# Kernel tuning notes

Hardware: AMD Instinct MI355X
Metric: run time of the kernel (lower is better)

The kernel has to match this reference:

```python
import jax, jax.numpy as jnp
import numpy as np

E = 8
HIDDEN = 1024
INTER = 4096
CAPS = np.array([512, 1024, 2048, 4096, 1024, 512, 2048, 1024], dtype=np.int64)  # sum = 12288
TOTAL = int(CAPS.sum())


def setup_inputs() -> dict:
    key = jax.random.key(0)
    k1, k2, k3, k4, k5 = jax.random.split(key, 5)
    s1 = 1.0 / np.sqrt(HIDDEN)
    s2 = 1.0 / np.sqrt(INTER)
    return {
        "inter_state": jax.random.normal(k1, (TOTAL, HIDDEN), dtype=jnp.float32),
        "w1": jax.random.normal(k2, (E, INTER, HIDDEN), dtype=jnp.float32) * s1,
        "b1": jax.random.normal(k3, (E, INTER), dtype=jnp.float32) * s1,
        "w2": jax.random.normal(k4, (E, HIDDEN, INTER), dtype=jnp.float32) * s2,
        "b2": jax.random.normal(k5, (E, HIDDEN), dtype=jnp.float32) * s2,
        "capacities": jnp.asarray(CAPS),
    }


def reference(inter_state, w1, b1, w2, b2, capacities):
    # Grouped GEMM: tokens are contiguous per expert with sizes = capacities.
    # Capacities are routing metadata (static for slicing).
    caps = np.asarray(capacities)
    offs = np.concatenate([[0], np.cumsum(caps)]).astype(np.int64)
    outs = []
    for e in range(caps.shape[0]):  # small fixed expert loop
        x = inter_state[int(offs[e]):int(offs[e + 1])]      # [cap_e, hidden]
        h = x @ w1[e].T + b1[e]                              # [cap_e, inter]
        outs.append(h @ w2[e].T + b2[e])                     # [cap_e, hidden]
    return jnp.concatenate(outs, axis=0)                     # [total, hidden]
```

## Files before the change

### kernel.cpp

```cpp
#include <hip/hip_runtime.h>
#include <hip/hip_bf16.h>

#define DEV __device__ __forceinline__

typedef __bf16 bf16x8 __attribute__((ext_vector_type(8)));
typedef float  f32x4  __attribute__((ext_vector_type(4)));


DEV unsigned short f2bf(float f) {
  union { float f; unsigned u; } v; v.f = f;
  unsigned u = v.u;
  return (unsigned short)((u + 0x7FFFu + ((u >> 16) & 1u)) >> 16);
}

DEV float bf2f(unsigned short s) {
  union { unsigned u; float f; } v; v.u = (unsigned)s << 16; return v.f;
}

DEV void gld_lds16(const void* g, void* l) {
  __builtin_amdgcn_global_load_lds(
      (const __attribute__((address_space(1))) unsigned int*)g,
      (__attribute__((address_space(3))) unsigned int*)l, 16, 0, 0);
}

#define WAITVM(N) asm volatile("s_waitcnt vmcnt(" #N ")" ::: "memory"); \
                  __builtin_amdgcn_sched_barrier(0)
#define WAITLG(N) asm volatile("s_waitcnt lgkmcnt(" #N ")" ::: "memory"); \
                  __builtin_amdgcn_sched_barrier(0)

template <int KT_, int KLEN, int SK, int N_, int NCT, bool OUT_BF16,
          bool HAS_BIAS, int EDIV>
__global__ __launch_bounds__(512, 2)
void gemm256(const unsigned short* __restrict__ A,
             const unsigned short* __restrict__ B,
             const float* __restrict__ bias,
             void* __restrict__ C0, void* __restrict__ C1) {
  __shared__ __align__(128) char lds[2][65536];
  constexpr int NTILES = KLEN / 64;

  const int tid  = threadIdx.x;
  const int lane = tid & 63;
  const int wv   = tid >> 6;
  const int wm   = wv >> 2;
  const int wn   = wv & 3;
  const int fr   = lane & 15;
  const int fq   = lane >> 4;

  int bid = blockIdx.x;
  const int nwg = gridDim.x;
  bid = (bid & 7) * (nwg >> 3) + (bid >> 3);

  int sk = 0;
  if constexpr (SK > 1) {
    const int per = nwg / SK;
    sk = bid / per;
    bid -= sk * per;
  }
  const int kStart = sk * KLEN;
  void* Cv = (SK > 1 && sk == 1) ? C1 : C0;

  const int rt = bid / NCT;
  const int ct = bid - rt * NCT;

  int e;
  if constexpr (EDIV > 0) {
    e = rt / EDIV;
  } else {
    const int cums[9] = {0, 2, 6, 14, 30, 34, 36, 44, 48};
    e = 0;
#pragma unroll
    for (int i = 1; i < 8; ++i) e += (rt >= cums[i]) ? 1 : 0;
  }

  const int grow0 = rt * 256;
  const int nloc0 = ct * 256;
  const unsigned short* Bg = B + (size_t)e * N_ * KT_;

  f32x4 acc[8][4];
#pragma unroll
  for (int i = 0; i < 8; ++i)
#pragma unroll
    for (int j = 0; j < 4; ++j) acc[i][j] = (f32x4){0.f, 0.f, 0.f, 0.f};

  auto stage_half = [&](int buf, int tk2, int h) {
    const int kb = kStart + tk2 * 64;
    char* dst = lds[buf] + h * 16384;
    const unsigned short* src = (h < 2) ? A : Bg;
    const int row0 = (h < 2) ? (grow0 + h * 128) : (nloc0 + (h - 2) * 128);
#pragma unroll
    for (int s = 0; s < 2; ++s) {
      int o  = s * 8192 + wv * 1024 + lane * 16;
      int r  = o >> 7;
      int cb = (o & 127) ^ ((r & 7) << 4);
      gld_lds16(src + (size_t)(row0 + r) * KT_ + kb + (cb >> 1),
                dst + s * 8192 + wv * 1024);
    }
  };

  stage_half(0, 0, 0); stage_half(0, 0, 1);
  stage_half(0, 0, 2); stage_half(0, 0, 3);

  const int brow0 = (wn & 1) * 64;

  for (int tk = 0; tk < NTILES; ++tk) {
    const int cur = tk & 1;
    WAITVM(0);
    __builtin_amdgcn_s_barrier();
    __builtin_amdgcn_sched_barrier(0);

    char* Ah = lds[cur] + wm * 16384;
    char* Bh = lds[cur] + (2 + (wn >> 1)) * 16384;
    const bool pre = (tk + 1 < NTILES);

    bf16x8 bfr[4][2], afr[2][2];
#pragma unroll
    for (int ni = 0; ni < 4; ++ni) {
      int r = brow0 + ni * 16 + fr;
#pragma unroll
      for (int k = 0; k < 2; ++k)
        bfr[ni][k] = *(bf16x8*)(Bh + r * 128 + ((k * 64 + fq * 16) ^ ((r & 7) << 4)));
    }
#pragma unroll
    for (int j = 0; j < 2; ++j) {
      int r = j * 16 + fr;
#pragma unroll
      for (int k = 0; k < 2; ++k)
        afr[j][k] = *(bf16x8*)(Ah + r * 128 + ((k * 64 + fq * 16) ^ ((r & 7) << 4)));
    }
    if (pre) { stage_half(cur ^ 1, tk + 1, 0); stage_half(cur ^ 1, tk + 1, 1); }
    WAITLG(0);
    __builtin_amdgcn_s_setprio(1);
#pragma unroll
    for (int k = 0; k < 2; ++k)
#pragma unroll
      for (int j = 0; j < 2; ++j)
#pragma unroll
        for (int ni = 0; ni < 4; ++ni)
          acc[j][ni] = __builtin_amdgcn_mfma_f32_16x16x32_bf16(
              afr[j][k], bfr[ni][k], acc[j][ni], 0, 0, 0);
    __builtin_amdgcn_s_setprio(0);

#pragma unroll
    for (int q = 1; q < 4; ++q) {
#pragma unroll
      for (int j = 0; j < 2; ++j) {
        int r = (2 * q + j) * 16 + fr;
#pragma unroll
        for (int k = 0; k < 2; ++k)
          afr[j][k] = *(bf16x8*)(Ah + r * 128 + ((k * 64 + fq * 16) ^ ((r & 7) << 4)));
      }
      if (q == 1 && pre) { stage_half(cur ^ 1, tk + 1, 2); stage_half(cur ^ 1, tk + 1, 3); }
      WAITLG(0);
      __builtin_amdgcn_s_setprio(1);
#pragma unroll
      for (int k = 0; k < 2; ++k)
#pragma unroll
        for (int j = 0; j < 2; ++j)
#pragma unroll
          for (int ni = 0; ni < 4; ++ni)
            acc[2 * q + j][ni] = __builtin_amdgcn_mfma_f32_16x16x32_bf16(
                afr[j][k], bfr[ni][k], acc[2 * q + j][ni], 0, 0, 0);
      __builtin_amdgcn_s_setprio(0);
    }
  }

#pragma unroll
  for (int ni = 0; ni < 4; ++ni) {
    int ncol = nloc0 + wn * 64 + ni * 16 + fr;
    float bv = 0.f;
    if constexpr (HAS_BIAS) bv = (bias + (size_t)e * N_)[ncol];
#pragma unroll
    for (int mi = 0; mi < 8; ++mi) {
      int m = grow0 + wm * 128 + mi * 16 + fq * 4;
#pragma unroll
      for (int j = 0; j < 4; ++j) {
        float val = acc[mi][ni][j] + bv;
        if constexpr (OUT_BF16)
          ((unsigned short*)Cv)[(size_t)(m + j) * N_ + ncol] = f2bf(val);
        else
          ((float*)Cv)[(size_t)(m + j) * N_ + ncol] = val;
      }
    }
  }
}

__global__ __launch_bounds__(256)
void reduce_bf16(const unsigned short* __restrict__ p0,
                 const unsigned short* __restrict__ p1,
                 unsigned short* __restrict__ out, int n8) {
  for (int i = blockIdx.x * 256 + threadIdx.x; i < n8; i += gridDim.x * 256) {
    ushort4 a0 = ((const ushort4*)p0)[2 * i];
    ushort4 a1 = ((const ushort4*)p0)[2 * i + 1];
    ushort4 b0 = ((const ushort4*)p1)[2 * i];
    ushort4 b1 = ((const ushort4*)p1)[2 * i + 1];
    ushort4 r0 = {f2bf(bf2f(a0.x) + bf2f(b0.x)), f2bf(bf2f(a0.y) + bf2f(b0.y)),
                  f2bf(bf2f(a0.z) + bf2f(b0.z)), f2bf(bf2f(a0.w) + bf2f(b0.w))};
    ushort4 r1 = {f2bf(bf2f(a1.x) + bf2f(b1.x)), f2bf(bf2f(a1.y) + bf2f(b1.y)),
                  f2bf(bf2f(a1.z) + bf2f(b1.z)), f2bf(bf2f(a1.w) + bf2f(b1.w))};
    ((ushort4*)out)[2 * i]     = r0;
    ((ushort4*)out)[2 * i + 1] = r1;
  }
}

DEV int swz(int r, int cbyte) {
  return (r * 64 + cbyte) ^ (((r >> 1) & 7) << 4);
}

template <int K_, int N_, bool OUT_BF16, bool HAS_BIAS, int EDIV>
__global__ __launch_bounds__(512, 2)
void gemm8(const unsigned short* __restrict__ A,
           const unsigned short* __restrict__ B,
           const float* __restrict__ bias, void* __restrict__ Cv) {
  __shared__ __align__(128) char lds[2][49152];
  const int t    = threadIdx.x;
  const int lane = t & 63;
  const int wv   = t >> 6;
  const int wm   = wv >> 1;
  const int wn   = wv & 1;
  const int fr   = lane & 15;
  const int fq   = lane >> 4;
  constexpr int NCT = N_ / 128;
  constexpr int NT  = K_ / 64;

  int bid = blockIdx.x;
  const int nwg = gridDim.x;
  bid = (bid & 7) * (nwg >> 3) + (bid >> 3);
  const int rt = bid / NCT;
  const int ct = bid - rt * NCT;

  int e;
  if constexpr (EDIV > 0) {
    e = rt / EDIV;
  } else {
    const int cums[9] = {0, 2, 6, 14, 30, 34, 36, 44, 48};
    e = 0;
#pragma unroll
    for (int i = 1; i < 8; ++i) e += (rt >= cums[i]) ? 1 : 0;
  }

  const int grow0 = rt * 256;
  const int nloc0 = ct * 128;
  const unsigned short* Bg = B + (size_t)e * N_ * K_;

  f32x4 acc[4][4];
#pragma unroll
  for (int i = 0; i < 4; ++i)
#pragma unroll
    for (int j = 0; j < 4; ++j) acc[i][j] = (f32x4){0.f, 0.f, 0.f, 0.f};

  auto stage = [&](int buf, int tk) {
    const int kb = tk * 64;
    char* Abase = lds[buf];
    char* Bbase = lds[buf] + 32768;
#pragma unroll
    for (int s = 0; s < 4; ++s) {
      int o  = s * 8192 + wv * 1024 + lane * 16;
      int r  = o >> 7;
      int cb = (o & 127) ^ ((r & 7) << 4);
      gld_lds16(A + (size_t)(grow0 + r) * K_ + kb + (cb >> 1),
                Abase + s * 8192 + wv * 1024);
    }
#pragma unroll
    for (int s = 0; s < 2; ++s) {
      int o  = s * 8192 + wv * 1024 + lane * 16;
      int r  = o >> 7;
      int cb = (o & 127) ^ ((r & 7) << 4);
      gld_lds16(Bg + (size_t)(nloc0 + r) * K_ + kb + (cb >> 1),
                Bbase + s * 8192 + wv * 1024);
    }
  };

  auto compute = [&](int buf) {
    char* Abase = lds[buf];
    char* Bbase = lds[buf] + 32768;
    bf16x8 af[4][2], bf[4][2];
#pragma unroll
    for (int mi = 0; mi < 4; ++mi) {
      int r = wm * 64 + mi * 16 + fr;
#pragma unroll
      for (int k = 0; k < 2; ++k)
        af[mi][k] = *(bf16x8*)(Abase + r * 128 + ((k * 64 + fq * 16) ^ ((r & 7) << 4)));
    }
#pragma unroll
    for (int ni = 0; ni < 4; ++ni) {
      int r = wn * 64 + ni * 16 + fr;
#pragma unroll
      for (int k = 0; k < 2; ++k)
        bf[ni][k] = *(bf16x8*)(Bbase + r * 128 + ((k * 64 + fq * 16) ^ ((r & 7) << 4)));
    }
    __builtin_amdgcn_s_setprio(1);
#pragma unroll
    for (int k = 0; k < 2; ++k)
#pragma unroll
      for (int mi = 0; mi < 4; ++mi)
#pragma unroll
        for (int ni = 0; ni < 4; ++ni)
          acc[mi][ni] = __builtin_amdgcn_mfma_f32_16x16x32_bf16(
              af[mi][k], bf[ni][k], acc[mi][ni], 0, 0, 0);
    __builtin_amdgcn_s_setprio(0);
  };

  stage(0, 0);
  for (int tk = 0; tk < NT; ++tk) {
    const int cur = tk & 1;
    if (tk + 1 < NT) {
      stage(cur ^ 1, tk + 1);
      WAITVM(6);
    } else {
      WAITVM(0);
    }
    __builtin_amdgcn_s_barrier();
    compute(cur);
    WAITLG(0);
    __builtin_amdgcn_s_barrier();
  }

#pragma unroll
  for (int ni = 0; ni < 4; ++ni) {
    int nloc = nloc0 + wn * 64 + ni * 16 + fr;
    float bv = 0.f;
    if constexpr (HAS_BIAS) bv = (bias + (size_t)e * N_)[nloc];
#pragma unroll
    for (int mi = 0; mi < 4; ++mi) {
      int m = grow0 + wm * 64 + mi * 16 + fq * 4;
#pragma unroll
      for (int j = 0; j < 4; ++j) {
        float val = acc[mi][ni][j] + bv;
        if constexpr (OUT_BF16)
          ((unsigned short*)Cv)[(size_t)(m + j) * N_ + nloc] = f2bf(val);
        else
          ((float*)Cv)[(size_t)(m + j) * N_ + nloc] = val;
      }
    }
  }
}

template <int K_, int N_, int NCT_, bool OUT_BF16, bool HAS_BIAS, int EDIV>
__global__ __launch_bounds__(256)
void gemm_expert(const void* __restrict__ Av, const void* __restrict__ Bv,
                 const float* __restrict__ bias, void* __restrict__ Cv) {
  __shared__ char lds[2][12288];
  const int t    = threadIdx.x;
  const int lane = t & 63;
  const int wv   = t >> 6;
  const int wr   = wv >> 1;
  const int wc   = wv & 1;
  const int fr   = lane & 15;
  const int fq   = lane >> 4;

  int bid = blockIdx.x;
  const int nwg = gridDim.x;
  if ((nwg & 7) == 0) bid = (bid & 7) * (nwg >> 3) + (bid >> 3);
  const int rt = bid / NCT_;
  const int ct = bid - rt * NCT_;

  int e;
  if constexpr (EDIV > 0) {
    e = rt / EDIV;
  } else {
    const int cums[9] = {0, 4, 12, 28, 60, 68, 72, 88, 96};
    e = 0;
#pragma unroll
    for (int i = 1; i < 8; ++i) e += (rt >= cums[i]) ? 1 : 0;
  }

  const int grow0 = rt * 128;
  const int nloc0 = ct * 64;

  f32x4 acc[4][2];
#pragma unroll
  for (int i = 0; i < 4; ++i)
#pragma unroll
    for (int j = 0; j < 2; ++j) acc[i][j] = (f32x4){0.f, 0.f, 0.f, 0.f};

  const float* Af = (const float*)Av;
  const unsigned short* Bb = (const unsigned short*)Bv + (size_t)e * N_ * K_;

  auto stage = [&](int buf, int kb) {
    char* As = lds[buf];
    char* Bs = lds[buf] + 8192;
#pragma unroll
    for (int it = 0; it < 4; ++it) {
      int q = t + it * 256, r = q >> 3, c = (q & 7) * 4;
      float4 f = *(const float4*)(Af + (size_t)(grow0 + r) * K_ + kb + c);
      ushort4 v = {f2bf(f.x), f2bf(f.y), f2bf(f.z), f2bf(f.w)};
      *(ushort4*)(As + swz(r, c * 2)) = v;
    }
    int o = wv * 1024 + lane * 16;
    int p = o ^ (((o >> 7) & 7) << 4);
    gld_lds16(Bb + (size_t)(nloc0 + (p >> 6)) * K_ + kb + ((p & 63) >> 1),
              Bs + wv * 1024);
  };

  auto compute = [&](int buf) {
    char* As = lds[buf];
    char* Bs = lds[buf] + 8192;
    bf16x8 af[4], bfg[2];
#pragma unroll
    for (int mi = 0; mi < 4; ++mi)
      af[mi] = *(bf16x8*)(As + swz(wr * 64 + mi * 16 + fr, fq * 16));
#pragma unroll
    for (int ni = 0; ni < 2; ++ni)
      bfg[ni] = *(bf16x8*)(Bs + swz(wc * 32 + ni * 16 + fr, fq * 16));
#pragma unroll
    for (int mi = 0; mi < 4; ++mi)
#pragma unroll
      for (int ni = 0; ni < 2; ++ni)
        acc[mi][ni] = __builtin_amdgcn_mfma_f32_16x16x32_bf16(
            af[mi], bfg[ni], acc[mi][ni], 0, 0, 0);
  };

  int cur = 0;
  stage(0, 0);
  __syncthreads();
  for (int kb = 32; kb < K_; kb += 32) {
    stage(cur ^ 1, kb);
    compute(cur);
    __syncthreads();
    cur ^= 1;
  }
  compute(cur);

#pragma unroll
  for (int ni = 0; ni < 2; ++ni) {
    int nloc = nloc0 + wc * 32 + ni * 16 + fr;
    float bv = 0.f;
    if constexpr (HAS_BIAS) bv = (bias + (size_t)e * N_)[nloc];
#pragma unroll
    for (int mi = 0; mi < 4; ++mi) {
      int m = grow0 + wr * 64 + mi * 16 + fq * 4;
#pragma unroll
      for (int j = 0; j < 4; ++j) {
        float val = acc[mi][ni][j] + bv;
        if constexpr (OUT_BF16)
          ((unsigned short*)Cv)[(size_t)(m + j) * N_ + nloc] = f2bf(val);
        else
          ((float*)Cv)[(size_t)(m + j) * N_ + nloc] = val;
      }
    }
  }
}

__global__ __launch_bounds__(256)
void transpose_w1(const float* __restrict__ w1, unsigned short* __restrict__ w1t) {
  __shared__ unsigned short tl[64 * 68];
  int b = blockIdx.x;
  int jt = b & 15, kt = (b >> 4) & 63, e = b >> 10;
  const float* src = w1 + ((size_t)e * 4096 + kt * 64) * 1024 + jt * 64;
  int t = threadIdx.x;
#pragma unroll
  for (int it = 0; it < 4; ++it) {
    int q = t + it * 256, kr = q >> 4, jc = (q & 15) * 4;
    float4 f = *(const float4*)(src + (size_t)kr * 1024 + jc);
    ushort4 v = {f2bf(f.x), f2bf(f.y), f2bf(f.z), f2bf(f.w)};
    *(ushort4*)&tl[kr * 68 + jc] = v;
  }
  __syncthreads();
  unsigned short* dst = w1t + ((size_t)e * 1024 + jt * 64) * 4096 + kt * 64;
#pragma unroll
  for (int it = 0; it < 4; ++it) {
    int q = t + it * 256, jr = q >> 4, kc = (q & 15) * 4;
    ushort4 v = {tl[(kc + 0) * 68 + jr], tl[(kc + 1) * 68 + jr],
                 tl[(kc + 2) * 68 + jr], tl[(kc + 3) * 68 + jr]};
    *(ushort4*)(dst + (size_t)jr * 4096 + kc) = v;
  }
}

template <bool STORE_BF>
__global__ __launch_bounds__(256)
void conv_w2_bias(const float* __restrict__ w2, const float* __restrict__ b1,
                  const float* __restrict__ b2, unsigned short* __restrict__ w2bf,
                  float* __restrict__ bc) {
  int row = blockIdx.x, e = row >> 10, t = threadIdx.x;
  const float* src = w2 + (size_t)row * 4096;
  const float* b1e = b1 + (size_t)e * 4096;
  float acc = 0.f;
#pragma unroll
  for (int it = 0; it < 4; ++it) {
    int c = (t + it * 256) * 4;
    float4 f = *(const float4*)(src + c);
    float4 g = *(const float4*)(b1e + c);
    acc += f.x * g.x + f.y * g.y + f.z * g.z + f.w * g.w;
    if constexpr (STORE_BF) {
      ushort4 v = {f2bf(f.x), f2bf(f.y), f2bf(f.z), f2bf(f.w)};
      *(ushort4*)(w2bf + (size_t)row * 4096 + c) = v;
    }
  }
#pragma unroll
  for (int o = 32; o > 0; o >>= 1) acc += __shfl_down(acc, o);
  __shared__ float red[4];
  if ((t & 63) == 0) red[t >> 6] = acc;
  __syncthreads();
  if (t == 0) bc[row] = red[0] + red[1] + red[2] + red[3] + b2[row];
}

__global__ __launch_bounds__(256)
void conv_f32_bf16(const float* __restrict__ in, unsigned short* __restrict__ out,
                   int n4) {
  for (int i = blockIdx.x * 256 + threadIdx.x; i < n4; i += gridDim.x * 256) {
    float4 f = *(const float4*)(in + (size_t)i * 4);
    ushort4 v = {f2bf(f.x), f2bf(f.y), f2bf(f.z), f2bf(f.w)};
    *(ushort4*)(out + (size_t)i * 4) = v;
  }
}

extern "C" void kernel_launch(void* const* d_in, const int* in_sizes, int n_in,
                              void* d_out, int out_size, void* d_ws, size_t ws_size,
                              hipStream_t stream) {
  const float* x  = (const float*)d_in[0];
  const float* w1 = (const float*)d_in[1];
  const float* b1 = (const float*)d_in[2];
  const float* w2 = (const float*)d_in[3];
  const float* b2 = (const float*)d_in[4];

  char* ws = (char*)d_ws;
  unsigned short* w1t = (unsigned short*)ws;
  const size_t NEED_T2 = 151126016, NEED_T3 = 176291840;

  if (ws_size >= NEED_T3) {
    unsigned short* w2bf = (unsigned short*)(ws + 67108864);
    unsigned short* Wc   = (unsigned short*)(ws + 134217728);
    float*          bc   = (float*)(ws + 150994944);
    unsigned short* xbf  = (unsigned short*)(ws + 151126016);
    unsigned short* p1   = xbf;

    transpose_w1<<<8192, 256, 0, stream>>>(w1, w1t);
    conv_w2_bias<true><<<8192, 256, 0, stream>>>(w2, b1, b2, w2bf, bc);
    gemm256<4096, 2048, 2, 1024, 4, true, false, 4>
        <<<256, 512, 0, stream>>>(w2bf, w1t, nullptr, Wc, p1);
    reduce_bf16<<<2048, 256, 0, stream>>>(Wc, p1, Wc, 8 * 1024 * 1024 / 8);
    conv_f32_bf16<<<2048, 256, 0, stream>>>(x, xbf, 12288 * 1024 / 4);
    gemm256<1024, 1024, 1, 1024, 4, false, true, 0>
        <<<192, 512, 0, stream>>>(xbf, Wc, bc, (float*)d_out, nullptr);
  } else if (ws_size >= NEED_T2) {
    unsigned short* w2bf = (unsigned short*)(ws + 67108864);
    unsigned short* Wc   = (unsigned short*)(ws + 134217728);
    float*          bc   = (float*)(ws + 150994944);

    transpose_w1<<<8192, 256, 0, stream>>>(w1, w1t);
    conv_w2_bias<true><<<8192, 256, 0, stream>>>(w2, b1, b2, w2bf, bc);
    gemm8<4096, 1024, true, false, 4>
        <<<256, 512, 0, stream>>>(w2bf, w1t, nullptr, Wc);
    gemm_expert<1024, 1024, 16, false, true, 0>
        <<<1536, 256, 0, stream>>>(x, Wc, bc, d_out);
  } else {
    unsigned short* Wc = (unsigned short*)(ws + 67108864);
    float*          bc = (float*)(ws + 83886080);

    transpose_w1<<<8192, 256, 0, stream>>>(w1, w1t);
    conv_w2_bias<false><<<8192, 256, 0, stream>>>(w2, b1, b2, nullptr, bc);
    gemm_expert<4096, 1024, 8, true, false, 8>
        <<<768, 256, 0, stream>>>(w2, w1t, nullptr, Wc);
    gemm_expert<1024, 1024, 16, false, true, 0>
        <<<1536, 256, 0, stream>>>(x, Wc, bc, d_out);
  }
}
```

Baseline: 205.0 us.

## Deepen GEMM prefetch pipeline with split A/B LDS buffers and partial waits

Reorganizes LDS into separate double-buffered A and B regions and prefetches B tiles two iterations ahead while A is prefetched one ahead. The per-iteration wait now uses a partial vmcnt instead of draining all loads, and a mid-iteration barrier lets the next tile's A overwrite safely. The intent is to hide global-load latency behind MFMA work in both GEMM stages, at the cost of an extra barrier per iteration and more complex buffer-reuse ordering.

```diff
diff --git a/kernel.cpp b/kernel.cpp
--- a/kernel.cpp
+++ b/kernel.cpp
@@ -27,16 +27,17 @@
                   __builtin_amdgcn_sched_barrier(0)
 #define WAITLG(N) asm volatile("s_waitcnt lgkmcnt(" #N ")" ::: "memory"); \
                   __builtin_amdgcn_sched_barrier(0)
+#define BARRIER() __builtin_amdgcn_s_barrier(); __builtin_amdgcn_sched_barrier(0)
 
 template <int KT_, int KLEN, int SK, int N_, int NCT, bool OUT_BF16,
           bool HAS_BIAS, int EDIV>
 __global__ __launch_bounds__(512, 2)
-void gemm256(const unsigned short* __restrict__ A,
-             const unsigned short* __restrict__ B,
-             const float* __restrict__ bias,
-             void* __restrict__ C0, void* __restrict__ C1) {
-  __shared__ __align__(128) char lds[2][65536];
-  constexpr int NTILES = KLEN / 64;
+void gemm256p(const unsigned short* __restrict__ A,
+              const unsigned short* __restrict__ B,
+              const float* __restrict__ bias,
+              void* __restrict__ C0, void* __restrict__ C1) {
+  __shared__ __align__(128) char lds[131072];
+  constexpr int NT = KLEN / 64;
 
   const int tid  = threadIdx.x;
   const int lane = tid & 63;
@@ -82,11 +83,11 @@
 #pragma unroll
     for (int j = 0; j < 4; ++j) acc[i][j] = (f32x4){0.f, 0.f, 0.f, 0.f};
 
-  auto stage_half = [&](int buf, int tk2, int h) {
-    const int kb = kStart + tk2 * 64;
-    char* dst = lds[buf] + h * 16384;
+  auto stage_half = [&](int t, int h) {
+    const int kb = kStart + t * 64;
+    char* dst = lds + (h >> 1) * 65536 + (t & 1) * 32768 + (h & 1) * 16384;
     const unsigned short* src = (h < 2) ? A : Bg;
-    const int row0 = (h < 2) ? (grow0 + h * 128) : (nloc0 + (h - 2) * 128);
+    const int row0 = (h < 2) ? (grow0 + (h & 1) * 128) : (nloc0 + (h & 1) * 128);
 #pragma unroll
     for (int s = 0; s < 2; ++s) {
       int o  = s * 8192 + wv * 1024 + lane * 16;
@@ -97,59 +98,66 @@
     }
   };
 
-  stage_half(0, 0, 0); stage_half(0, 0, 1);
-  stage_half(0, 0, 2); stage_half(0, 0, 3);
+  stage_half(0, 0); stage_half(0, 1); stage_half(0, 2); stage_half(0, 3);
+  if constexpr (NT > 1) { stage_half(1, 2); stage_half(1, 3); }
 
   const int brow0 = (wn & 1) * 64;
 
-  for (int tk = 0; tk < NTILES; ++tk) {
-    const int cur = tk & 1;
-    WAITVM(0);
-    __builtin_amdgcn_s_barrier();
-    __builtin_amdgcn_sched_barrier(0);
-
-    char* Ah = lds[cur] + wm * 16384;
-    char* Bh = lds[cur] + (2 + (wn >> 1)) * 16384;
-    const bool pre = (tk + 1 < NTILES);
-
-    bf16x8 bfr[4][2], afr[2][2];
-#pragma unroll
-    for (int ni = 0; ni < 4; ++ni) {
-      int r = brow0 + ni * 16 + fr;
+  for (int t = 0; t < NT; ++t) {
+    char* Ah = lds + (t & 1) * 32768 + wm * 16384;
+    char* Bh = lds + 65536 + (t & 1) * 32768 + ((wn >> 1) * 16384);
+
+    if (t + 1 < NT) { WAITVM(4); } else { WAITVM(0); }
+    BARRIER();
+
+    bf16x8 bfr[4][2];
+    {
+      bf16x8 af[2][2];
+#pragma unroll
+      for (int ni = 0; ni < 4; ++ni) {
+        int r = brow0 + ni * 16 + fr;
+#pragma unroll
+        for (int k = 0; k < 2; ++k)
+          bfr[ni][k] = *(bf16x8*)(Bh + r * 128 + ((k * 64 + fq * 16) ^ ((r & 7) << 4)));
+      }
+#pragma unroll
+      for (int j = 0; j < 2; ++j) {
+        int r = j * 16 + fr;
+#pragma unroll
+        for (int k = 0; k < 2; ++k)
+          af[j][k] = *(bf16x8*)(Ah + r * 128 + ((k * 64 + fq * 16) ^ ((r & 7) << 4)));
+      }
+      if (t + 1 < NT) stage_half(t + 1, 0);
+      WAITLG(0);
+      __builtin_amdgcn_s_setprio(1);
 #pragma unroll
       for (int k = 0; k < 2; ++k)
-        bfr[ni][k] = *(bf16x8*)(Bh + r * 128 + ((k * 64 + fq * 16) ^ ((r & 7) << 4)));
-    }
-#pragma unroll
-    for (int j = 0; j < 2; ++j) {
-      int r = j * 16 + fr;
-#pragma unroll
-      for (int k = 0; k < 2; ++k)
-        afr[j][k] = *(bf16x8*)(Ah + r * 128 + ((k * 64 + fq * 16) ^ ((r & 7) << 4)));
-    }
-    if (pre) { stage_half(cur ^ 1, tk + 1, 0); stage_half(cur ^ 1, tk + 1, 1); }
-    WAITLG(0);
-    __builtin_amdgcn_s_setprio(1);
-#pragma unroll
-    for (int k = 0; k < 2; ++k)
-#pragma unroll
-      for (int j = 0; j < 2; ++j)
-#pragma unroll
-        for (int ni = 0; ni < 4; ++ni)
-          acc[j][ni] = __builtin_amdgcn_mfma_f32_16x16x32_bf16(
-              afr[j][k], bfr[ni][k], acc[j][ni], 0, 0, 0);
-    __builtin_amdgcn_s_setprio(0);
+#pragma unroll
+        for (int j = 0; j < 2; ++j)
+#pragma unroll
+          for (int ni = 0; ni < 4; ++ni)
+            acc[j][ni] = __builtin_amdgcn_mfma_f32_16x16x32_bf16(
+                af[j][k], bfr[ni][k], acc[j][ni], 0, 0, 0);
+      __builtin_amdgcn_s_setprio(0);
+      BARRIER();
+    }
 
 #pragma unroll
     for (int q = 1; q < 4; ++q) {
+      bf16x8 af[2][2];
 #pragma unroll
       for (int j = 0; j < 2; ++j) {
         int r = (2 * q + j) * 16 + fr;
 #pragma unroll
         for (int k = 0; k < 2; ++k)
-          afr[j][k] = *(bf16x8*)(Ah + r * 128 + ((k * 64 + fq * 16) ^ ((r & 7) << 4)));
-      }
-      if (q == 1 && pre) { stage_half(cur ^ 1, tk + 1, 2); stage_half(cur ^ 1, tk + 1, 3); }
+          af[j][k] = *(bf16x8*)(Ah + r * 128 + ((k * 64 + fq * 16) ^ ((r & 7) << 4)));
+      }
+      if (q == 1) {
+        if (t + 1 < NT) stage_half(t + 1, 1);
+        if (t + 2 < NT) stage_half(t + 2, 2);
+      } else if (q == 2) {
+        if (t + 2 < NT) stage_half(t + 2, 3);
+      }
       WAITLG(0);
       __builtin_amdgcn_s_setprio(1);
 #pragma unroll
@@ -159,7 +167,7 @@
 #pragma unroll
           for (int ni = 0; ni < 4; ++ni)
             acc[2 * q + j][ni] = __builtin_amdgcn_mfma_f32_16x16x32_bf16(
-                afr[j][k], bfr[ni][k], acc[2 * q + j][ni], 0, 0, 0);
+                af[j][k], bfr[ni][k], acc[2 * q + j][ni], 0, 0, 0);
       __builtin_amdgcn_s_setprio(0);
     }
   }
@@ -526,11 +534,11 @@
 
     transpose_w1<<<8192, 256, 0, stream>>>(w1, w1t);
     conv_w2_bias<true><<<8192, 256, 0, stream>>>(w2, b1, b2, w2bf, bc);
-    gemm256<4096, 2048, 2, 1024, 4, true, false, 4>
+    gemm256p<4096, 2048, 2, 1024, 4, true, false, 4>
         <<<256, 512, 0, stream>>>(w2bf, w1t, nullptr, Wc, p1);
     reduce_bf16<<<2048, 256, 0, stream>>>(Wc, p1, Wc, 8 * 1024 * 1024 / 8);
     conv_f32_bf16<<<2048, 256, 0, stream>>>(x, xbf, 12288 * 1024 / 4);
-    gemm256<1024, 1024, 1, 1024, 4, false, true, 0>
+    gemm256p<1024, 1024, 1, 1024, 4, false, true, 0>
         <<<192, 512, 0, stream>>>(xbf, Wc, bc, (float*)d_out, nullptr);
   } else if (ws_size >= NEED_T2) {
     unsigned short* w2bf = (unsigned short*)(ws + 67108864);
```

Measured after the change: 202.8 us. No clear change (-1.1%).
